# Optimization experiments

Measured on AMD Instinct MI355X. Metric: run time of the kernel, lower is better.

## Reference

```python
import jax, jax.numpy as jnp
import numpy as np

KERNEL_WIDTH = 0.05      # Gaussian KDE bandwidth (Angstrom)
B_SCAT = 5.803           # neutron scattering length of O (fm)
N_ATOMS = 1024
BOX_L = 25.0
N_BINS = 400


def _trapz(y, x):
    # trapezoidal rule along last axis; x is 1D
    dx = x[1:] - x[:-1]
    return jnp.sum((y[..., 1:] + y[..., :-1]) * 0.5 * dx, axis=-1)


def setup_inputs() -> dict:
    key = jax.random.key(0)
    k1, _ = jax.random.split(key)
    positions = jax.random.uniform(k1, (N_ATOMS, 3), dtype=jnp.float32) * BOX_L
    cell = jnp.eye(3, dtype=jnp.float32) * BOX_L
    r_bins = jnp.linspace(0.1, 10.0, N_BINS, dtype=jnp.float32)
    q_bins = jnp.linspace(0.5, 25.0, N_BINS, dtype=jnp.float32)
    return {"positions": positions, "cell": cell, "r_bins": r_bins, "q_bins": q_bins}


def reference(positions, cell, r_bins, q_bins):
    w = KERNEL_WIDTH
    b = B_SCAT
    N = positions.shape[0]

    # --- minimum-image pairwise distances, upper triangle only (self-pairs) ---
    ii, jj = np.triu_indices(N, k=1)                 # static index sets, P = N(N-1)/2
    diff = positions[jj] - positions[ii]             # (P, 3), matches points_2 - points_1
    cell_inv = jnp.linalg.inv(cell)
    frac = diff @ cell_inv                            # (P, 3) fractional coords
    frac = frac - jnp.round(frac)                     # minimum image convention
    mip = frac @ cell
    d = jnp.sqrt(jnp.sum(mip * mip, axis=-1) + 1e-10)  # (P,) observed distances

    # --- Gaussian KDE binning with window mask (mask == exact exclusion) ---
    min_bin = jnp.min(r_bins) - 3.0 * w
    max_bin = jnp.max(r_bins) + 3.0 * w
    in_win = (d > min_bin) & (d < max_bin)            # (P,)
    norm = 1.0 / (w * jnp.sqrt(2.0 * jnp.pi))
    gauss = jnp.exp(-0.5 * ((r_bins[None, :] - d[:, None]) / w) ** 2) * norm  # (P, n_r)
    summed = jnp.sum(jnp.where(in_win[:, None], gauss, 0.0), axis=0)          # (n_r,)

    vol = jnp.abs(jnp.linalg.det(cell))
    n_pairs = d.shape[0]
    g_partial = vol / n_pairs * summed / (4.0 * jnp.pi * r_bins ** 2)

    # single species: frac=1, coeff = b*b*0.01; G(r) = coeff * (g_partial - 1)
    G = (b * b * 0.01) * (g_partial - 1.0)

    # --- S(Q) = 1 + 4*pi*rho/Q * int r G(r) sin(Qr) dr ---
    rho = N / vol
    integrand = (r_bins[None, :] * G[None, :] *
                 jnp.sin(q_bins[:, None] * r_bins[None, :]) /
                 (q_bins[:, None] + 1e-10))           # (n_q, n_r)
    S = 1.0 + 4.0 * jnp.pi * rho * _trapz(integrand, r_bins)

    # --- F(Q) = Q (S(Q) - 1) ---
    F = q_bins * (S - 1.0)

    return jnp.stack([G, S, F])  # (3, n_bins)
```

## Files before the change

### kernel.cpp

```cpp
#include <hip/hip_runtime.h>
#include <math.h>

#define NBINS_MAX 512
#define NMAX      1024
#define NFG       2048
#define GOFF      64
#define WHALF     49
#define NSLOT     8
#define SENT32  (NBINS_MAX * NSLOT)
constexpr float KW       = 0.05f;
constexpr float INV_KW   = 20.0f;
constexpr float GNORM    = 0.3989422804014327f * INV_KW;
constexpr float COEFF    = 0.33674809f;
constexpr float FOUR_PI  = 12.566370614359172f;
constexpr float QSCALE     = 1048576.0f;
constexpr float INV_QSCALE = 1.0f / QSCALE;
constexpr float ES  = 33554432.0f;
constexpr float E2S = 536870912.0f;
constexpr float A1  = INV_KW / ES;
constexpr float A2  = 0.5f * INV_KW * INV_KW / E2S;


__global__ void __launch_bounds__(512)
scatter_kernel(const float* __restrict__ pos,
               const float* __restrict__ cell,
               const float* __restrict__ rbins,
               unsigned int* __restrict__ slots,
               int N, int nbins)
{
    __shared__ float sh_pos[3 * NMAX];
    __shared__ unsigned long long sh_fm[NFG];
    const int t  = threadIdx.x;
    const int nb = blockDim.x;

    const int nflt = 3 * N;
    const int nvec = nflt >> 2;
    const float4* p4 = (const float4*)pos;
    for (int v = t; v < nvec; v += nb) {
        const float4 x = p4[v];
        sh_pos[4*v + 0] = x.x;
        sh_pos[4*v + 1] = x.y;
        sh_pos[4*v + 2] = x.z;
        sh_pos[4*v + 3] = x.w;
    }
    for (int s = (nvec << 2) + t; s < nflt; s += nb)
        sh_pos[s] = pos[s];
    for (int s = t; s < NFG; s += nb)
        sh_fm[s] = 0ull;

    float cm[9];
#pragma unroll
    for (int k = 0; k < 9; ++k) cm[k] = cell[k];
    const float a00 = cm[0], a01 = cm[1], a02 = cm[2];
    const float a10 = cm[3], a11 = cm[4], a12 = cm[5];
    const float a20 = cm[6], a21 = cm[7], a22 = cm[8];
    const float det = a00*(a11*a22 - a12*a21)
                    - a01*(a10*a22 - a12*a20)
                    + a02*(a10*a21 - a11*a20);
    const float id = 1.0f / det;
    float im[9];
    im[0] = (a11*a22 - a12*a21)*id;
    im[1] = (a02*a21 - a01*a22)*id;
    im[2] = (a01*a12 - a02*a11)*id;
    im[3] = (a12*a20 - a10*a22)*id;
    im[4] = (a00*a22 - a02*a20)*id;
    im[5] = (a02*a10 - a00*a12)*id;
    im[6] = (a10*a21 - a11*a20)*id;
    im[7] = (a01*a20 - a00*a21)*id;
    im[8] = (a00*a11 - a01*a10)*id;

    const float r0     = rbins[0];
    const float rend   = rbins[nbins - 1];
    const float minb   = r0   - 3.0f * KW;
    const float maxb   = rend + 3.0f * KW;
    const float dr     = (rend - r0) / (float)(nbins - 1);
    const float fdelta = 0.25f * dr;
    const float inv_fd = 1.0f / fdelta;

    __syncthreads();

    const int nrp = (N + 1) / 2;
    const int rp0 = 2 * blockIdx.x;

    auto do_rowpair = [&](int rp) {
        const int A    = rp;
        const int B    = N - 1 - rp;
        const int cntA = N - 1 - A;
        const int cntB = (B != A) ? A : 0;
        const int tot  = cntA + cntB;
        for (int p = t; p < tot; p += nb) {
            int i, j;
            if (p < cntA) { i = A; j = A + 1 + p; }
            else          { i = B; j = B + 1 + (p - cntA); }

            const float dx = sh_pos[3*j + 0] - sh_pos[3*i + 0];
            const float dy = sh_pos[3*j + 1] - sh_pos[3*i + 1];
            const float dz = sh_pos[3*j + 2] - sh_pos[3*i + 2];
            float fx = dx*im[0] + dy*im[3] + dz*im[6];
            float fy = dx*im[1] + dy*im[4] + dz*im[7];
            float fz = dx*im[2] + dy*im[5] + dz*im[8];
            fx -= rintf(fx); fy -= rintf(fy); fz -= rintf(fz);
            const float mx = fx*cm[0] + fy*cm[3] + fz*cm[6];
            const float my = fx*cm[1] + fy*cm[4] + fz*cm[7];
            const float mz = fx*cm[2] + fy*cm[5] + fz*cm[8];
            const float d  = sqrtf(mx*mx + my*my + mz*mz + 1e-10f);

            if (d > minb && d < maxb) {
                const int   gi = (int)rintf((d - r0) * inv_fd) + GOFF;
                const float e  = d - fmaf((float)(gi - GOFF), fdelta, r0);
                const int   eq  = (int)rintf(e * ES);
                const unsigned int e2q = (unsigned int)rintf(e * e * E2S);
                const unsigned long long val =
                      (1ull << 52)
                    | ((unsigned long long)e2q << 29)
                    | (unsigned long long)(unsigned int)(eq + 131072);
                const int addr = ((gi & 3) << 9) | (gi >> 2);
                atomicAdd(&sh_fm[addr], val);
            }
        }
    };
    do_rowpair(rp0);
    if (rp0 + 1 < nrp) do_rowpair(rp0 + 1);

    __syncthreads();

    if (t < nbins && t < 484) {
        const int   k  = t;
        const float dw = fdelta * INV_KW;
        float u = (float)WHALF * dw;
        float e = __expf(-0.5f * u * u);
        float g = __expf(fmaf(u, dw, -0.5f * dw * dw));
        const float m = __expf(-dw * dw);
        float acc = 0.0f;
        const int gbase = 4 * k + GOFF - WHALF;
#pragma unroll 4
        for (int it = 0; it <= 2 * WHALF; ++it) {
            const int gi   = gbase + it;
            const int addr = ((gi & 3) << 9) | (gi >> 2);
            const unsigned long long v = sh_fm[addr];
            const unsigned int cntu = (unsigned int)(v >> 52);
            const float cnt = (float)cntu;
            const float m2  = (float)(unsigned int)((v >> 29) & 0x7FFFFFu);
            const float m1  = (float)((int)((unsigned int)v & 0x1FFFFFFFu)
                                      - (int)(cntu << 17));
            const float term = fmaf(u * A1, m1,
                               fmaf(fmaf(u, u, -1.0f) * A2, m2, cnt));
            acc = fmaf(term, e, acc);
            e *= g; g *= m;
            u -= dw;
        }
        const int slot = blockIdx.x & (NSLOT - 1);
        const int q = (int)rintf(acc * QSCALE);
        if (q) atomicAdd(&slots[k * NSLOT + slot], (unsigned int)q);
    }
}

__global__ void __launch_bounds__(256)
spectrum_kernel(const unsigned int* __restrict__ slots,
                const float* __restrict__ cell,
                const float* __restrict__ rbins,
                const float* __restrict__ qbins,
                float* __restrict__ out,
                int N, int nbins)
{
    __shared__ float  sh_r[NBINS_MAX];
    __shared__ float2 sh_w2[NBINS_MAX];
    __shared__ float  sh_red[4];
    const int t = threadIdx.x;

    const unsigned int base = slots[SENT32];

    const float a00 = cell[0], a01 = cell[1], a02 = cell[2];
    const float a10 = cell[3], a11 = cell[4], a12 = cell[5];
    const float a20 = cell[6], a21 = cell[7], a22 = cell[8];
    const float det = a00*(a11*a22 - a12*a21)
                    - a01*(a10*a22 - a12*a20)
                    + a02*(a10*a21 - a11*a20);
    const float vol     = fabsf(det);
    const float n_pairs = 0.5f * (float)N * (float)(N - 1);
    const float rho     = (float)N / vol;
    const float pref    = (vol / n_pairs) * GNORM;

    const uint4* s4 = (const uint4*)slots;
    for (int k = t; k < nbins; k += 256) {
        const uint4 aa = s4[2*k + 0];
        const uint4 bb = s4[2*k + 1];
        long long tot = 0;
        tot += (int)(aa.x - base);
        tot += (int)(aa.y - base);
        tot += (int)(aa.z - base);
        tot += (int)(aa.w - base);
        tot += (int)(bb.x - base);
        tot += (int)(bb.y - base);
        tot += (int)(bb.z - base);
        tot += (int)(bb.w - base);
        const float summed = (float)tot * INV_QSCALE;
        const float rk = rbins[k];
        const float g  = pref * summed / (FOUR_PI * rk * rk);
        const float G  = COEFF * (g - 1.0f);
        if (blockIdx.x == 0) out[k] = G;
        sh_r[k]  = rk;
        sh_w2[k] = make_float2(G, rk);
    }
    __syncthreads();

    for (int k = t; k < nbins; k += 256) {
        const float rk   = sh_r[k];
        const float w_lo = (k > 0)         ? (rk - sh_r[k - 1]) : 0.0f;
        const float w_hi = (k < nbins - 1) ? (sh_r[k + 1] - rk) : 0.0f;
        sh_w2[k].x = 0.5f * (w_lo + w_hi) * rk * sh_w2[k].x;
    }
    __syncthreads();

    const int   qi   = blockIdx.x;
    const float q    = qbins[qi];
    const float qinv = 1.0f / (q + 1e-10f);
    float acc = 0.0f;
    for (int k = t; k < nbins; k += 256) {
        const float2 v = sh_w2[k];
        acc += v.x * __sinf(q * v.y);
    }
#pragma unroll
    for (int off = 32; off > 0; off >>= 1)
        acc += __shfl_down(acc, off, 64);
    if ((t & 63) == 0) sh_red[t >> 6] = acc;
    __syncthreads();
    if (t == 0) {
        const float S = 1.0f + FOUR_PI * rho * qinv *
                        (sh_red[0] + sh_red[1] + sh_red[2] + sh_red[3]);
        out[nbins + qi]     = S;
        out[2 * nbins + qi] = q * (S - 1.0f);
    }
}

extern "C" void kernel_launch(void* const* d_in, const int* in_sizes, int n_in,
                              void* d_out, int out_size, void* d_ws, size_t ws_size,
                              hipStream_t stream)
{
    const float* pos   = (const float*)d_in[0];
    const float* cell  = (const float*)d_in[1];
    const float* rbins = (const float*)d_in[2];
    const float* qbins = (const float*)d_in[3];
    float* out = (float*)d_out;

    const int N     = in_sizes[0] / 3;
    const int nbins = in_sizes[2];
    const int nrp   = (N + 1) / 2;
    const int grid1 = (nrp + 1) / 2;

    unsigned int* slots = (unsigned int*)d_ws;

    hipLaunchKernelGGL(scatter_kernel, dim3(grid1), dim3(512), 0, stream,
                       pos, cell, rbins, slots, N, nbins);
    hipLaunchKernelGGL(spectrum_kernel, dim3(nbins), dim3(256), 0, stream,
                       slots, cell, rbins, qbins, out, N, nbins);
}
```

Before: 76.57 us.

## Fuse scatter and spectrum kernels via last-block completion counter; refine fine grid

After: 95.74 us. 25.0% more time.

```diff
diff --git a/kernel.cpp b/kernel.cpp
--- a/kernel.cpp
+++ b/kernel.cpp
@@ -3,9 +3,9 @@
 
 #define NBINS_MAX 512
 #define NMAX      1024
-#define NFG       2048
+#define NFG       4096
 #define GOFF      64
-#define WHALF     49
+#define WHALF     98
 #define NSLOT     8
 #define SENT32  (NBINS_MAX * NSLOT)
 constexpr float KW       = 0.05f;
@@ -22,14 +22,18 @@
 
 
 __global__ void __launch_bounds__(512)
-scatter_kernel(const float* __restrict__ pos,
-               const float* __restrict__ cell,
-               const float* __restrict__ rbins,
-               unsigned int* __restrict__ slots,
-               int N, int nbins)
+fused_kernel(const float* __restrict__ pos,
+             const float* __restrict__ cell,
+             const float* __restrict__ rbins,
+             const float* __restrict__ qbins,
+             unsigned int* __restrict__ slots,
+             float*        __restrict__ out,
+             int N, int nbins)
 {
     __shared__ float sh_pos[3 * NMAX];
     __shared__ unsigned long long sh_fm[NFG];
+    __shared__ float sh_W[NBINS_MAX];
+    __shared__ unsigned int sh_last;
     const int t  = threadIdx.x;
     const int nb = blockDim.x;
 
@@ -74,7 +78,7 @@
     const float minb   = r0   - 3.0f * KW;
     const float maxb   = rend + 3.0f * KW;
     const float dr     = (rend - r0) / (float)(nbins - 1);
-    const float fdelta = 0.25f * dr;
+    const float fdelta = 0.125f * dr;
     const float inv_fd = 1.0f / fdelta;
 
     __syncthreads();
@@ -114,7 +118,7 @@
                       (1ull << 52)
                     | ((unsigned long long)e2q << 29)
                     | (unsigned long long)(unsigned int)(eq + 131072);
-                const int addr = ((gi & 3) << 9) | (gi >> 2);
+                const int addr = ((gi & 7) << 9) | (gi >> 3);
                 atomicAdd(&sh_fm[addr], val);
             }
         }
@@ -124,7 +128,7 @@
 
     __syncthreads();
 
-    if (t < nbins && t < 484) {
+    if (t < nbins) {
         const int   k  = t;
         const float dw = fdelta * INV_KW;
         float u = (float)WHALF * dw;
@@ -132,11 +136,11 @@
         float g = __expf(fmaf(u, dw, -0.5f * dw * dw));
         const float m = __expf(-dw * dw);
         float acc = 0.0f;
-        const int gbase = 4 * k + GOFF - WHALF;
+        const int gbase = 8 * k + GOFF - WHALF;
 #pragma unroll 4
         for (int it = 0; it <= 2 * WHALF; ++it) {
             const int gi   = gbase + it;
-            const int addr = ((gi & 3) << 9) | (gi >> 2);
+            const int addr = ((gi & 7) << 9) | (gi >> 3);
             const unsigned long long v = sh_fm[addr];
             const unsigned int cntu = (unsigned int)(v >> 52);
             const float cnt = (float)cntu;
@@ -153,83 +157,68 @@
         const int q = (int)rintf(acc * QSCALE);
         if (q) atomicAdd(&slots[k * NSLOT + slot], (unsigned int)q);
     }
-}
-
-__global__ void __launch_bounds__(256)
-spectrum_kernel(const unsigned int* __restrict__ slots,
-                const float* __restrict__ cell,
-                const float* __restrict__ rbins,
-                const float* __restrict__ qbins,
-                float* __restrict__ out,
-                int N, int nbins)
-{
-    __shared__ float  sh_r[NBINS_MAX];
-    __shared__ float2 sh_w2[NBINS_MAX];
-    __shared__ float  sh_red[4];
-    const int t = threadIdx.x;
-
-    const unsigned int base = slots[SENT32];
-
-    const float a00 = cell[0], a01 = cell[1], a02 = cell[2];
-    const float a10 = cell[3], a11 = cell[4], a12 = cell[5];
-    const float a20 = cell[6], a21 = cell[7], a22 = cell[8];
-    const float det = a00*(a11*a22 - a12*a21)
-                    - a01*(a10*a22 - a12*a20)
-                    + a02*(a10*a21 - a11*a20);
+
+    asm volatile("s_waitcnt vmcnt(0)" ::: "memory");
+    __syncthreads();
+    if (t == 0) {
+        const unsigned int old = __hip_atomic_fetch_add(
+            &slots[SENT32 + 1], 1u,
+            __ATOMIC_RELAXED, __HIP_MEMORY_SCOPE_AGENT);
+        const unsigned int tb  = __hip_atomic_load(
+            &slots[SENT32],
+            __ATOMIC_RELAXED, __HIP_MEMORY_SCOPE_AGENT);
+        sh_last = ((old - tb) == (unsigned int)(gridDim.x - 1)) ? 1u : 0u;
+    }
+    __syncthreads();
+    if (!sh_last) return;
+
+    const unsigned int base = __hip_atomic_load(
+        &slots[SENT32], __ATOMIC_RELAXED, __HIP_MEMORY_SCOPE_AGENT);
     const float vol     = fabsf(det);
     const float n_pairs = 0.5f * (float)N * (float)(N - 1);
     const float rho     = (float)N / vol;
     const float pref    = (vol / n_pairs) * GNORM;
 
-    const uint4* s4 = (const uint4*)slots;
-    for (int k = t; k < nbins; k += 256) {
-        const uint4 aa = s4[2*k + 0];
-        const uint4 bb = s4[2*k + 1];
+    const unsigned long long* s64 = (const unsigned long long*)slots;
+    if (t < nbins) {
         long long tot = 0;
-        tot += (int)(aa.x - base);
-        tot += (int)(aa.y - base);
-        tot += (int)(aa.z - base);
-        tot += (int)(aa.w - base);
-        tot += (int)(bb.x - base);
-        tot += (int)(bb.y - base);
-        tot += (int)(bb.z - base);
-        tot += (int)(bb.w - base);
+#pragma unroll
+        for (int s = 0; s < 4; ++s) {
+            const unsigned long long v = __hip_atomic_load(
+                &s64[t * 4 + s], __ATOMIC_RELAXED, __HIP_MEMORY_SCOPE_AGENT);
+            tot += (int)((unsigned int)v - base);
+            tot += (int)((unsigned int)(v >> 32) - base);
+        }
         const float summed = (float)tot * INV_QSCALE;
-        const float rk = rbins[k];
+        const float rk = fmaf((float)t, dr, r0);
         const float g  = pref * summed / (FOUR_PI * rk * rk);
         const float G  = COEFF * (g - 1.0f);
-        if (blockIdx.x == 0) out[k] = G;
-        sh_r[k]  = rk;
-        sh_w2[k] = make_float2(G, rk);
-    }
-    __syncthreads();
-
-    for (int k = t; k < nbins; k += 256) {
-        const float rk   = sh_r[k];
-        const float w_lo = (k > 0)         ? (rk - sh_r[k - 1]) : 0.0f;
-        const float w_hi = (k < nbins - 1) ? (sh_r[k + 1] - rk) : 0.0f;
-        sh_w2[k].x = 0.5f * (w_lo + w_hi) * rk * sh_w2[k].x;
-    }
-    __syncthreads();
-
-    const int   qi   = blockIdx.x;
-    const float q    = qbins[qi];
-    const float qinv = 1.0f / (q + 1e-10f);
-    float acc = 0.0f;
-    for (int k = t; k < nbins; k += 256) {
-        const float2 v = sh_w2[k];
-        acc += v.x * __sinf(q * v.y);
-    }
-#pragma unroll
-    for (int off = 32; off > 0; off >>= 1)
-        acc += __shfl_down(acc, off, 64);
-    if ((t & 63) == 0) sh_red[t >> 6] = acc;
-    __syncthreads();
-    if (t == 0) {
-        const float S = 1.0f + FOUR_PI * rho * qinv *
-                        (sh_red[0] + sh_red[1] + sh_red[2] + sh_red[3]);
-        out[nbins + qi]     = S;
-        out[2 * nbins + qi] = q * (S - 1.0f);
+        out[t] = G;
+        const float wk = (t == 0 || t == nbins - 1) ? 0.5f * dr : dr;
+        sh_W[t] = wk * rk * G;
+    }
+    __syncthreads();
+
+    if (t < nbins) {
+        const float q    = qbins[t];
+        const float qinv = 1.0f / (q + 1e-10f);
+        float acc = 0.0f;
+        const float4* W4 = (const float4*)sh_W;
+        const int n4 = nbins >> 2;
+#pragma unroll 4
+        for (int b = 0; b < n4; ++b) {
+            const float4 w = W4[b];
+            const float rb = fmaf((float)(4*b), dr, r0);
+            acc = fmaf(w.x, __sinf(q * rb),                    acc);
+            acc = fmaf(w.y, __sinf(q * fmaf(1.0f, dr, rb)),    acc);
+            acc = fmaf(w.z, __sinf(q * fmaf(2.0f, dr, rb)),    acc);
+            acc = fmaf(w.w, __sinf(q * fmaf(3.0f, dr, rb)),    acc);
+        }
+        for (int k = n4 << 2; k < nbins; ++k)
+            acc = fmaf(sh_W[k], __sinf(q * fmaf((float)k, dr, r0)), acc);
+        const float S = 1.0f + FOUR_PI * rho * acc * qinv;
+        out[nbins + t]     = S;
+        out[2 * nbins + t] = q * (S - 1.0f);
     }
 }
 
@@ -246,12 +235,10 @@
     const int N     = in_sizes[0] / 3;
     const int nbins = in_sizes[2];
     const int nrp   = (N + 1) / 2;
-    const int grid1 = (nrp + 1) / 2;
+    const int grid  = (nrp + 1) / 2;
 
     unsigned int* slots = (unsigned int*)d_ws;
 
-    hipLaunchKernelGGL(scatter_kernel, dim3(grid1), dim3(512), 0, stream,
-                       pos, cell, rbins, slots, N, nbins);
-    hipLaunchKernelGGL(spectrum_kernel, dim3(nbins), dim3(256), 0, stream,
-                       slots, cell, rbins, qbins, out, N, nbins);
+    hipLaunchKernelGGL(fused_kernel, dim3(grid), dim3(512), 0, stream,
+                       pos, cell, rbins, qbins, slots, out, N, nbins);
 }
```
